# Kernel tuning notes

Hardware: AMD Instinct MI355X
Metric: run time of the kernel (lower is better)

Reference implementation:

```python
import jax, jax.numpy as jnp
import numpy as np

N_EMB = 1024
N_HEAD = 16
HEAD_SIZE = N_EMB // N_HEAD  # 64
B, T = 4, 4096


def setup_inputs() -> dict:
    key = jax.random.key(0)
    kx, kq, kk, kv = jax.random.split(key, 4)
    x = jax.random.normal(kx, (B, T, N_EMB), dtype=jnp.float32)
    # torch nn.Linear(in=N_EMB, out=HEAD_SIZE, bias=False) weight: [out, in]
    s = 1.0 / np.sqrt(N_EMB)
    Wq = jax.random.uniform(kq, (HEAD_SIZE, N_EMB), jnp.float32, -s, s)
    Wk = jax.random.uniform(kk, (HEAD_SIZE, N_EMB), jnp.float32, -s, s)
    Wv = jax.random.uniform(kv, (HEAD_SIZE, N_EMB), jnp.float32, -s, s)
    return {"x": x, "Wq": Wq, "Wk": Wk, "Wv": Wv}


def reference(x, Wq, Wk, Wv):
    # q,k,v: [B,T,H]
    q = jnp.einsum('btc,hc->bth', x, Wq)
    k = jnp.einsum('btc,hc->bth', x, Wk)
    v = jnp.einsum('btc,hc->bth', x, Wv)
    scale = HEAD_SIZE ** (-0.5)
    att = jnp.einsum('bth,bsh->bts', q, k) * scale  # [B,T,T]
    Tn = x.shape[1]
    causal = jnp.tril(jnp.ones((Tn, Tn), dtype=bool))
    att = jnp.where(causal, att, -jnp.inf)
    att = jax.nn.softmax(att, axis=-1)
    # dropout p=0.0 -> identity
    out = jnp.einsum('bts,bsh->bth', att, v)  # [B,T,H]
    return out
```

## Files before the change

### kernel.cpp

```cpp
#include <hip/hip_runtime.h>


typedef __attribute__((ext_vector_type(8))) short v8s;
typedef __attribute__((ext_vector_type(4))) float v4f;

static __device__ __forceinline__ unsigned short f2bf(float x) {
  unsigned int u = __builtin_bit_cast(unsigned int, x);
  u += 0x7fffu + ((u >> 16) & 1u);
  return (unsigned short)(u >> 16);
}

static __device__ __forceinline__ void dma16(const void* src, void* dst) {
  __builtin_amdgcn_global_load_lds(
      (const __attribute__((address_space(1))) void*)src,
      (__attribute__((address_space(3))) void*)dst, 16, 0, 0);
}

__global__ __launch_bounds__(256) void pack_w(const float* __restrict__ Wq,
                                              const float* __restrict__ Wk,
                                              const float* __restrict__ Wv,
                                              unsigned short* __restrict__ WF) {
  int idx = (blockIdx.x * 256 + threadIdx.x) * 4;
  int row = idx >> 10;
  int k   = idx & 1023;
  const float* src;
  float scale;
  if (row < 64)       { src = Wq + row * 1024 + k;         scale = 0.125f; }
  else if (row < 128) { src = Wk + (row - 64) * 1024 + k;  scale = 1.0f;   }
  else                { src = Wv + (row - 128) * 1024 + k; scale = 1.0f;   }
  float4 f = *(const float4*)src;
  ushort4 o;
  o.x = f2bf(f.x * scale); o.y = f2bf(f.y * scale);
  o.z = f2bf(f.z * scale); o.w = f2bf(f.w * scale);
  size_t off = ((size_t)(k >> 5) * 12 + (row >> 4)) * 512 +
               (((k >> 3) & 3) * 16 + (row & 15)) * 8 + (k & 7);
  *(ushort4*)(WF + off) = o;
}

__global__ __launch_bounds__(256) void qkv(const float* __restrict__ x,
                                           const unsigned short* __restrict__ WF,
                                           unsigned short* __restrict__ Qg,
                                           unsigned short* __restrict__ KF,
                                           unsigned short* __restrict__ VF) {
  __shared__ alignas(16) char xs[2][16384];
  const int tid   = threadIdx.x;
  const int lane  = tid & 63;
  const int wv    = tid >> 6;
  const int quad  = lane >> 4;
  const int colid = lane & 15;
  const int row0  = blockIdx.x * 32;

  const char* xB = (const char*)x;
  const unsigned short* wf = WF + lane * 8;

  const int rpar = lane >> 5;
  const int su_l = lane & 31;
  const int c7   = colid & 7;

  v4f acc[6];
#pragma unroll
  for (int i = 0; i < 6; i++) acc[i] = (v4f){0.f, 0.f, 0.f, 0.f};

  auto stage = [&](int kt, int slot) {
#pragma unroll
    for (int i = 0; i < 4; i++) {
      int j    = wv * 4 + i;
      int rloc = 2 * j + rpar;
      int u    = su_l ^ (rloc & 7);
      const char* src = xB + (size_t)(row0 + rloc) * 4096 + kt * 512 + u * 16;
      dma16(src, &xs[slot][j * 1024]);
    }
  };

  stage(0, 0);

  for (int kt = 0; kt < 8; kt++) {
    const int slot = kt & 1;
    __syncthreads();
    if (kt < 7) stage(kt + 1, slot ^ 1);
#pragma unroll
    for (int s = 0; s < 4; s++) {
      const int g = kt * 4 + s;
      v8s bw[3];
#pragma unroll
      for (int ntl = 0; ntl < 3; ntl++)
        bw[ntl] = *(const v8s*)(wf + ((size_t)g * 12 + wv * 3 + ntl) * 512);
#pragma unroll
      for (int mg = 0; mg < 2; mg++) {
        const int rr = mg * 16 + colid;
        const int u0 = s * 8 + quad * 2;
        float4 f0 = *(const float4*)(&xs[slot][rr * 512 + (u0 ^ c7) * 16]);
        float4 f1 = *(const float4*)(&xs[slot][rr * 512 + ((u0 + 1) ^ c7) * 16]);
        v8s a;
        a[0] = (short)f2bf(f0.x); a[1] = (short)f2bf(f0.y);
        a[2] = (short)f2bf(f0.z); a[3] = (short)f2bf(f0.w);
        a[4] = (short)f2bf(f1.x); a[5] = (short)f2bf(f1.y);
        a[6] = (short)f2bf(f1.z); a[7] = (short)f2bf(f1.w);
#pragma unroll
        for (int ntl = 0; ntl < 3; ntl++)
          acc[mg * 3 + ntl] =
              __builtin_amdgcn_mfma_f32_16x16x32_bf16(a, bw[ntl], acc[mg * 3 + ntl], 0, 0, 0);
      }
    }
  }

#pragma unroll
  for (int ntl = 0; ntl < 3; ntl++) {
    const int nt = wv * 3 + ntl;
#pragma unroll
    for (int mg = 0; mg < 2; mg++) {
      const int trow_base = row0 + mg * 16 + quad * 4;
      if (nt < 4) {
#pragma unroll
        for (int r = 0; r < 4; r++)
          Qg[(size_t)(trow_base + r) * 64 + nt * 16 + colid] =
              f2bf(acc[mg * 3 + ntl][r]);
      } else if (nt < 8) {
        int half = (nt - 4) >> 1;
        int q_f  = ((nt - 4) * 2 + (colid >> 3)) & 3;
        int j    = colid & 7;
#pragma unroll
        for (int r = 0; r < 4; r++) {
          int t  = trow_base + r;
          int b  = t >> 12, tl = t & 4095;
          int si = tl >> 6, sl = tl & 63;
          KF[((size_t)(b * 64 + si) * 8 + (sl >> 4) * 2 + half) * 512 +
             (q_f * 16 + (sl & 15)) * 8 + j] = f2bf(acc[mg * 3 + ntl][r]);
        }
      } else {
#pragma unroll
        for (int r = 0; r < 4; r++) {
          int t  = trow_base + r;
          int b  = t >> 12, tl = t & 4095;
          int si = tl >> 6;
          int half = (tl >> 5) & 1, q_f = (tl >> 3) & 3, j = tl & 7;
          VF[((size_t)(b * 64 + si) * 8 + (nt - 8) * 2 + half) * 512 +
             (q_f * 16 + colid) * 8 + j] = f2bf(acc[mg * 3 + ntl][r]);
        }
      }
    }
  }
}

__global__ __launch_bounds__(256, 2) void flash(const unsigned short* __restrict__ Qg,
                                                const unsigned short* __restrict__ KF,
                                                const unsigned short* __restrict__ VF,
                                                float* __restrict__ out) {
  __shared__ alignas(16) char smem[4 * 32 * 68 * 4 + 4 * 32 * 4];
  unsigned short* pl = (unsigned short*)smem;
  float* redf = (float*)smem;
  float* lred = (float*)(smem + 4 * 32 * 68 * 4);

  const int tid   = threadIdx.x;
  const int lane  = tid & 63;
  const int wv    = tid >> 6;
  const int quad  = lane >> 4;
  const int colid = lane & 15;
  const int qt32  = 127 - (int)(blockIdx.x >> 2);
  const int b     = blockIdx.x & 3;
  const int bT    = b * 4096;
  const int row00 = qt32 * 32;
  const int qimax = (row00 + 31) >> 6;

  v8s qf[2][2];
#pragma unroll
  for (int mt = 0; mt < 2; mt++) {
    const unsigned short* qrow =
        Qg + (size_t)(bT + row00 + mt * 16 + colid) * 64 + quad * 8;
    qf[mt][0] = *(const v8s*)(qrow);
    qf[mt][1] = *(const v8s*)(qrow + 32);
  }

  v8s ones;
#pragma unroll
  for (int j = 0; j < 8; j++) ones[j] = (short)0x3F80;

  v4f o[2][4];
#pragma unroll
  for (int mt = 0; mt < 2; mt++)
#pragma unroll
    for (int i = 0; i < 4; i++) o[mt][i] = (v4f){0.f, 0.f, 0.f, 0.f};
  v4f lac[2];
  lac[0] = (v4f){0.f, 0.f, 0.f, 0.f};
  lac[1] = (v4f){0.f, 0.f, 0.f, 0.f};

  const unsigned short* kb0 = KF + (size_t)b * 64 * 4096 + lane * 8;
  const unsigned short* vb0 = VF + (size_t)b * 64 * 4096 + lane * 8;

  for (int si = wv; si <= qimax; si += 4) {
    const unsigned short* ktile = kb0 + (size_t)si * 4096;
    const unsigned short* vtile = vb0 + (size_t)si * 4096;
    v8s ck[8], cv[8];
#pragma unroll
    for (int c = 0; c < 8; c++) ck[c] = *(const v8s*)(ktile + (size_t)c * 512);
#pragma unroll
    for (int c = 0; c < 8; c++) cv[c] = *(const v8s*)(vtile + (size_t)c * 512);

#pragma unroll
    for (int mt = 0; mt < 2; mt++) {
      v4f s[4];
#pragma unroll
      for (int i = 0; i < 4; i++) s[i] = (v4f){0.f, 0.f, 0.f, 0.f};
#pragma unroll
      for (int nt = 0; nt < 4; nt++) {
        s[nt] = __builtin_amdgcn_mfma_f32_16x16x32_bf16(qf[mt][0], ck[2 * nt], s[nt], 0, 0, 0);
        s[nt] = __builtin_amdgcn_mfma_f32_16x16x32_bf16(qf[mt][1], ck[2 * nt + 1], s[nt], 0, 0, 0);
      }

      if (si == qimax) {
        int rowb = row00 + mt * 16 + quad * 4;
        int colb = si * 64;
#pragma unroll
        for (int nt = 0; nt < 4; nt++)
#pragma unroll
          for (int r = 0; r < 4; r++)
            if (colb + nt * 16 + colid > rowb + r) s[nt][r] = -1e30f;
      }

      unsigned short* pw = pl + (wv * 2 + mt) * (16 * 72);
#pragma unroll
      for (int nt = 0; nt < 4; nt++)
#pragma unroll
        for (int r = 0; r < 4; r++)
          pw[(quad * 4 + r) * 72 + nt * 16 + colid] = f2bf(__expf(s[nt][r]));
    }

#pragma unroll
    for (int mt = 0; mt < 2; mt++) {
      unsigned short* pw = pl + (wv * 2 + mt) * (16 * 72);
#pragma unroll
      for (int ks = 0; ks < 64; ks += 32) {
        v8s af = *(const v8s*)(&pw[colid * 72 + ks + quad * 8]);
        lac[mt] = __builtin_amdgcn_mfma_f32_16x16x32_bf16(af, ones, lac[mt], 0, 0, 0);
#pragma unroll
        for (int nt = 0; nt < 4; nt++)
          o[mt][nt] = __builtin_amdgcn_mfma_f32_16x16x32_bf16(
              af, cv[2 * nt + (ks >> 5)], o[mt][nt], 0, 0, 0);
      }
    }
  }

  __syncthreads();
#pragma unroll
  for (int mt = 0; mt < 2; mt++) {
#pragma unroll
    for (int nt = 0; nt < 4; nt++)
#pragma unroll
      for (int r = 0; r < 4; r++)
        redf[(wv * 32 + mt * 16 + quad * 4 + r) * 68 + nt * 16 + colid] = o[mt][nt][r];
    if (colid == 0) {
#pragma unroll
      for (int r = 0; r < 4; r++)
        lred[wv * 32 + mt * 16 + quad * 4 + r] = lac[mt][r];
    }
  }
  __syncthreads();

  {
    int col = tid & 63;
    int r0  = tid >> 6;
#pragma unroll
    for (int rr = 0; rr < 8; rr++) {
      int row = r0 * 8 + rr;
      float sum = 0.f, lsum = 0.f;
#pragma unroll
      for (int w = 0; w < 4; w++) {
        sum  += redf[(w * 32 + row) * 68 + col];
        lsum += lred[w * 32 + row];
      }
      out[(size_t)(bT + row00 + row) * 64 + col] = sum / lsum;
    }
  }
}

extern "C" void kernel_launch(void* const* d_in, const int* in_sizes, int n_in,
                              void* d_out, int out_size, void* d_ws, size_t ws_size,
                              hipStream_t stream) {
  const float* x  = (const float*)d_in[0];
  const float* Wq = (const float*)d_in[1];
  const float* Wk = (const float*)d_in[2];
  const float* Wv = (const float*)d_in[3];
  float* out = (float*)d_out;

  unsigned short* WF = (unsigned short*)d_ws;
  unsigned short* Qg = WF + 192 * 1024;
  unsigned short* KF = Qg + 16384 * 64;
  unsigned short* VF = KF + 16384 * 64;

  hipLaunchKernelGGL(pack_w, dim3(192), dim3(256), 0, stream, Wq, Wk, Wv, WF);
  hipLaunchKernelGGL(qkv, dim3(512), dim3(256), 0, stream, x, WF, Qg, KF, VF);
  hipLaunchKernelGGL(flash, dim3(512), dim3(256), 0, stream, Qg, KF, VF, out);
}
```

Baseline: 132.2 us.

## Halve qkv row tile and use eight waves per flash block

The QKV projection now gives each block 16 rows instead of 32, which doubles the grid to 1024 blocks and halves accumulators and LDS per block. The flash kernel now runs 512 threads (8 waves), with each wave taking every eighth key tile, and the cross-wave reduction becomes a two-stage tree through LDS. Both changes aim to raise parallelism and occupancy on the causal-attention workload. In exchange, qkv loses weight reuse across two row groups, and flash adds extra synchronisation steps and a serial final reduction in wave 0.

```diff
diff --git a/kernel.cpp b/kernel.cpp
--- a/kernel.cpp
+++ b/kernel.cpp
@@ -42,13 +42,13 @@
                                            unsigned short* __restrict__ Qg,
                                            unsigned short* __restrict__ KF,
                                            unsigned short* __restrict__ VF) {
-  __shared__ alignas(16) char xs[2][16384];
+  __shared__ alignas(16) char xs[2][8192];
   const int tid   = threadIdx.x;
   const int lane  = tid & 63;
   const int wv    = tid >> 6;
   const int quad  = lane >> 4;
   const int colid = lane & 15;
-  const int row0  = blockIdx.x * 32;
+  const int row0  = blockIdx.x * 16;
 
   const char* xB = (const char*)x;
   const unsigned short* wf = WF + lane * 8;
@@ -57,14 +57,14 @@
   const int su_l = lane & 31;
   const int c7   = colid & 7;
 
-  v4f acc[6];
-#pragma unroll
-  for (int i = 0; i < 6; i++) acc[i] = (v4f){0.f, 0.f, 0.f, 0.f};
+  v4f acc[3];
+#pragma unroll
+  for (int i = 0; i < 3; i++) acc[i] = (v4f){0.f, 0.f, 0.f, 0.f};
 
   auto stage = [&](int kt, int slot) {
 #pragma unroll
-    for (int i = 0; i < 4; i++) {
-      int j    = wv * 4 + i;
+    for (int i = 0; i < 2; i++) {
+      int j    = wv * 2 + i;
       int rloc = 2 * j + rpar;
       int u    = su_l ^ (rloc & 7);
       const char* src = xB + (size_t)(row0 + rloc) * 4096 + kt * 512 + u * 16;
@@ -85,68 +85,59 @@
 #pragma unroll
       for (int ntl = 0; ntl < 3; ntl++)
         bw[ntl] = *(const v8s*)(wf + ((size_t)g * 12 + wv * 3 + ntl) * 512);
-#pragma unroll
-      for (int mg = 0; mg < 2; mg++) {
-        const int rr = mg * 16 + colid;
-        const int u0 = s * 8 + quad * 2;
-        float4 f0 = *(const float4*)(&xs[slot][rr * 512 + (u0 ^ c7) * 16]);
-        float4 f1 = *(const float4*)(&xs[slot][rr * 512 + ((u0 + 1) ^ c7) * 16]);
-        v8s a;
-        a[0] = (short)f2bf(f0.x); a[1] = (short)f2bf(f0.y);
-        a[2] = (short)f2bf(f0.z); a[3] = (short)f2bf(f0.w);
-        a[4] = (short)f2bf(f1.x); a[5] = (short)f2bf(f1.y);
-        a[6] = (short)f2bf(f1.z); a[7] = (short)f2bf(f1.w);
-#pragma unroll
-        for (int ntl = 0; ntl < 3; ntl++)
-          acc[mg * 3 + ntl] =
-              __builtin_amdgcn_mfma_f32_16x16x32_bf16(a, bw[ntl], acc[mg * 3 + ntl], 0, 0, 0);
-      }
-    }
-  }
-
+      const int u0 = s * 8 + quad * 2;
+      float4 f0 = *(const float4*)(&xs[slot][colid * 512 + (u0 ^ c7) * 16]);
+      float4 f1 = *(const float4*)(&xs[slot][colid * 512 + ((u0 + 1) ^ c7) * 16]);
+      v8s a;
+      a[0] = (short)f2bf(f0.x); a[1] = (short)f2bf(f0.y);
+      a[2] = (short)f2bf(f0.z); a[3] = (short)f2bf(f0.w);
+      a[4] = (short)f2bf(f1.x); a[5] = (short)f2bf(f1.y);
+      a[6] = (short)f2bf(f1.z); a[7] = (short)f2bf(f1.w);
+#pragma unroll
+      for (int ntl = 0; ntl < 3; ntl++)
+        acc[ntl] = __builtin_amdgcn_mfma_f32_16x16x32_bf16(a, bw[ntl], acc[ntl], 0, 0, 0);
+    }
+  }
+
+  const int trow_base = row0 + quad * 4;
 #pragma unroll
   for (int ntl = 0; ntl < 3; ntl++) {
     const int nt = wv * 3 + ntl;
-#pragma unroll
-    for (int mg = 0; mg < 2; mg++) {
-      const int trow_base = row0 + mg * 16 + quad * 4;
-      if (nt < 4) {
-#pragma unroll
-        for (int r = 0; r < 4; r++)
-          Qg[(size_t)(trow_base + r) * 64 + nt * 16 + colid] =
-              f2bf(acc[mg * 3 + ntl][r]);
-      } else if (nt < 8) {
-        int half = (nt - 4) >> 1;
-        int q_f  = ((nt - 4) * 2 + (colid >> 3)) & 3;
-        int j    = colid & 7;
-#pragma unroll
-        for (int r = 0; r < 4; r++) {
-          int t  = trow_base + r;
-          int b  = t >> 12, tl = t & 4095;
-          int si = tl >> 6, sl = tl & 63;
-          KF[((size_t)(b * 64 + si) * 8 + (sl >> 4) * 2 + half) * 512 +
-             (q_f * 16 + (sl & 15)) * 8 + j] = f2bf(acc[mg * 3 + ntl][r]);
-        }
-      } else {
-#pragma unroll
-        for (int r = 0; r < 4; r++) {
-          int t  = trow_base + r;
-          int b  = t >> 12, tl = t & 4095;
-          int si = tl >> 6;
-          int half = (tl >> 5) & 1, q_f = (tl >> 3) & 3, j = tl & 7;
-          VF[((size_t)(b * 64 + si) * 8 + (nt - 8) * 2 + half) * 512 +
-             (q_f * 16 + colid) * 8 + j] = f2bf(acc[mg * 3 + ntl][r]);
-        }
-      }
-    }
-  }
-}
-
-__global__ __launch_bounds__(256, 2) void flash(const unsigned short* __restrict__ Qg,
-                                                const unsigned short* __restrict__ KF,
-                                                const unsigned short* __restrict__ VF,
-                                                float* __restrict__ out) {
-  __shared__ alignas(16) char smem[4 * 32 * 68 * 4 + 4 * 32 * 4];
+    if (nt < 4) {
+#pragma unroll
+      for (int r = 0; r < 4; r++)
+        Qg[(size_t)(trow_base + r) * 64 + nt * 16 + colid] = f2bf(acc[ntl][r]);
+    } else if (nt < 8) {
+      int half = (nt - 4) >> 1;
+      int q_f  = ((nt - 4) * 2 + (colid >> 3)) & 3;
+      int j    = colid & 7;
+#pragma unroll
+      for (int r = 0; r < 4; r++) {
+        int t  = trow_base + r;
+        int b  = t >> 12, tl = t & 4095;
+        int si = tl >> 6, sl = tl & 63;
+        KF[((size_t)(b * 64 + si) * 8 + (sl >> 4) * 2 + half) * 512 +
+           (q_f * 16 + (sl & 15)) * 8 + j] = f2bf(acc[ntl][r]);
+      }
+    } else {
+#pragma unroll
+      for (int r = 0; r < 4; r++) {
+        int t  = trow_base + r;
+        int b  = t >> 12, tl = t & 4095;
+        int si = tl >> 6;
+        int half = (tl >> 5) & 1, q_f = (tl >> 3) & 3, j = tl & 7;
+        VF[((size_t)(b * 64 + si) * 8 + (nt - 8) * 2 + half) * 512 +
+           (q_f * 16 + colid) * 8 + j] = f2bf(acc[ntl][r]);
+      }
+    }
+  }
+}
+
+__global__ __launch_bounds__(512) void flash(const unsigned short* __restrict__ Qg,
+                                             const unsigned short* __restrict__ KF,
+                                             const unsigned short* __restrict__ VF,
+                                             float* __restrict__ out) {
+  __shared__ alignas(16) char smem[8 * 2 * 16 * 72 * 2];
   unsigned short* pl = (unsigned short*)smem;
   float* redf = (float*)smem;
   float* lred = (float*)(smem + 4 * 32 * 68 * 4);
@@ -187,7 +178,7 @@
   const unsigned short* kb0 = KF + (size_t)b * 64 * 4096 + lane * 8;
   const unsigned short* vb0 = VF + (size_t)b * 64 * 4096 + lane * 8;
 
-  for (int si = wv; si <= qimax; si += 4) {
+  for (int si = wv; si <= qimax; si += 8) {
     const unsigned short* ktile = kb0 + (size_t)si * 4096;
     const unsigned short* vtile = vb0 + (size_t)si * 4096;
     v8s ck[8], cv[8];
@@ -241,35 +232,70 @@
   }
 
   __syncthreads();
-#pragma unroll
-  for (int mt = 0; mt < 2; mt++) {
-#pragma unroll
-    for (int nt = 0; nt < 4; nt++)
+  if (wv >= 4) {
+    int slot = wv - 4;
+#pragma unroll
+    for (int mt = 0; mt < 2; mt++) {
+#pragma unroll
+      for (int nt = 0; nt < 4; nt++)
+#pragma unroll
+        for (int r = 0; r < 4; r++)
+          redf[(slot * 32 + mt * 16 + quad * 4 + r) * 68 + nt * 16 + colid] = o[mt][nt][r];
+      if (colid == 0) {
+#pragma unroll
+        for (int r = 0; r < 4; r++)
+          lred[slot * 32 + mt * 16 + quad * 4 + r] = lac[mt][r];
+      }
+    }
+  }
+  __syncthreads();
+  if (wv < 4) {
+#pragma unroll
+    for (int mt = 0; mt < 2; mt++) {
+#pragma unroll
+      for (int nt = 0; nt < 4; nt++)
+#pragma unroll
+        for (int r = 0; r < 4; r++)
+          o[mt][nt][r] += redf[(wv * 32 + mt * 16 + quad * 4 + r) * 68 + nt * 16 + colid];
 #pragma unroll
       for (int r = 0; r < 4; r++)
-        redf[(wv * 32 + mt * 16 + quad * 4 + r) * 68 + nt * 16 + colid] = o[mt][nt][r];
-    if (colid == 0) {
-#pragma unroll
-      for (int r = 0; r < 4; r++)
-        lred[wv * 32 + mt * 16 + quad * 4 + r] = lac[mt][r];
+        lac[mt][r] += lred[wv * 32 + mt * 16 + quad * 4 + r];
     }
   }
   __syncthreads();
-
-  {
-    int col = tid & 63;
-    int r0  = tid >> 6;
-#pragma unroll
-    for (int rr = 0; rr < 8; rr++) {
-      int row = r0 * 8 + rr;
-      float sum = 0.f, lsum = 0.f;
-#pragma unroll
-      for (int w = 0; w < 4; w++) {
-        sum  += redf[(w * 32 + row) * 68 + col];
-        lsum += lred[w * 32 + row];
-      }
-      out[(size_t)(bT + row00 + row) * 64 + col] = sum / lsum;
-    }
+  if (wv >= 1 && wv < 4) {
+    int slot = wv - 1;
+#pragma unroll
+    for (int mt = 0; mt < 2; mt++) {
+#pragma unroll
+      for (int nt = 0; nt < 4; nt++)
+#pragma unroll
+        for (int r = 0; r < 4; r++)
+          redf[(slot * 32 + mt * 16 + quad * 4 + r) * 68 + nt * 16 + colid] = o[mt][nt][r];
+      if (colid == 0) {
+#pragma unroll
+        for (int r = 0; r < 4; r++)
+          lred[slot * 32 + mt * 16 + quad * 4 + r] = lac[mt][r];
+      }
+    }
+  }
+  __syncthreads();
+  if (wv == 0) {
+#pragma unroll
+    for (int mt = 0; mt < 2; mt++)
+#pragma unroll
+      for (int r = 0; r < 4; r++) {
+        int row = mt * 16 + quad * 4 + r;
+        float lsum = lac[mt][r] + lred[row] + lred[32 + row] + lred[64 + row];
+        float inv = 1.0f / lsum;
+#pragma unroll
+        for (int nt = 0; nt < 4; nt++) {
+          float sum = o[mt][nt][r] + redf[row * 68 + nt * 16 + colid] +
+                      redf[(32 + row) * 68 + nt * 16 + colid] +
+                      redf[(64 + row) * 68 + nt * 16 + colid];
+          out[(size_t)(bT + row00 + row) * 64 + nt * 16 + colid] = sum * inv;
+        }
+      }
   }
 }
 
@@ -288,6 +314,6 @@
   unsigned short* VF = KF + 16384 * 64;
 
   hipLaunchKernelGGL(pack_w, dim3(192), dim3(256), 0, stream, Wq, Wk, Wv, WF);
-  hipLaunchKernelGGL(qkv, dim3(512), dim3(256), 0, stream, x, WF, Qg, KF, VF);
-  hipLaunchKernelGGL(flash, dim3(512), dim3(256), 0, stream, Qg, KF, VF, out);
-}
+  hipLaunchKernelGGL(qkv, dim3(1024), dim3(256), 0, stream, x, WF, Qg, KF, VF);
+  hipLaunchKernelGGL(flash, dim3(512), dim3(512), 0, stream, Qg, KF, VF, out);
+}
```

Result: slower. 136.4 us (+3.2%).
